# Kernel optimization log

Hardware: AMD Instinct MI355X
Metric: run time of the kernel (lower is better)

The kernel has to match this reference:

```python
import jax, jax.numpy as jnp
import numpy as np
from jax import lax

# Fixed-point scales (powers of two, as in linger's luna/venus pipeline).
# scale_gi = input_scale * weight_ih_scale, scale_gh = hidden_scale * weight_hh_scale.
SCALE_GI = 2.0 ** 14
SCALE_GH = 2.0 ** 14
Q27 = 2.0 ** 27
Q15 = 2.0 ** 15
Q31 = 2.0 ** 31
INT32_MIN = -(2.0 ** 31)
INT32_MAX = 2.0 ** 31 - 1


def quant_round(x, scale):
    # QuantMode.floor_add: floor(x*scale + 0.5)/scale, with straight-through gradient
    # (linger QAT rounding uses STE).
    q = jnp.floor(x * scale + 0.5) / scale
    return x + lax.stop_gradient(q - x)


@jax.custom_vjp
def qsigmoid(x):
    # Quantize input to Q27 int32, evaluate sigmoid, output Q31 -> requant to Q15.
    i_q27 = jnp.clip(jnp.floor(x * Q27 + 0.5), INT32_MIN, INT32_MAX)
    s = jax.nn.sigmoid(i_q27 / Q27)
    out_q31 = jnp.floor(s * Q31 + 0.5)
    out_q15 = jnp.floor(out_q31 * (2.0 ** -16) + 0.5)  # luna_requant(31 -> 15)
    return out_q15 / Q15

def _qsig_fwd(x):
    return qsigmoid(x), x

def _qsig_bwd(x, g):
    s = jax.nn.sigmoid(x)
    return (g * s * (1.0 - s),)

qsigmoid.defvjp(_qsig_fwd, _qsig_bwd)


@jax.custom_vjp
def qtanh(x):
    i_q27 = jnp.clip(jnp.floor(x * Q27 + 0.5), INT32_MIN, INT32_MAX)
    t = jnp.tanh(i_q27 / Q27)
    out_q31 = jnp.floor(t * Q31 + 0.5)
    out_q15 = jnp.floor(out_q31 * (2.0 ** -16) + 0.5)
    return out_q15 / Q15

def _qtanh_fwd(x):
    return qtanh(x), x

def _qtanh_bwd(x, g):
    t = jnp.tanh(x)
    return (g * (1.0 - t * t),)

qtanh.defvjp(_qtanh_fwd, _qtanh_bwd)


def setup_inputs() -> dict:
    key = jax.random.key(0)
    k = jax.random.split(key, 6)
    B, I, H = 8192, 512, 512
    return {
        "input_x": jax.random.normal(k[0], (B, I), dtype=jnp.float32),
        "hidden": jax.random.normal(k[1], (B, H), dtype=jnp.float32),
        "weight_ih": jax.random.normal(k[2], (3 * H, I), dtype=jnp.float32) * 0.05,
        "weight_hh": jax.random.normal(k[3], (3 * H, H), dtype=jnp.float32) * 0.05,
        "bias_ih": jax.random.normal(k[4], (3 * H,), dtype=jnp.float32) * 0.05,
        "bias_hh": jax.random.normal(k[5], (3 * H,), dtype=jnp.float32) * 0.05,
    }


def reference(input_x, hidden, weight_ih, weight_hh, bias_ih, bias_hh):
    # Dense gate projections: [B, 3H]
    gi = input_x @ weight_ih.T + bias_ih
    gh = hidden @ weight_hh.T + bias_hh
    # Requant gate pre-activations to fixed-point grid (biasih/biashh quantizers)
    gi = quant_round(gi, SCALE_GI)
    gh = quant_round(gh, SCALE_GH)
    i_r, i_i, i_n = jnp.split(gi, 3, axis=1)
    h_r, h_i, h_n = jnp.split(gh, 3, axis=1)
    resetgate = qsigmoid(i_r + h_r)
    inputgate = qsigmoid(i_i + h_i)
    # h_n requantized to Q27, reset*h_n product requantized to Q15
    h_n = quant_round(h_n, Q27)
    resetgate_h_n = quant_round(resetgate * h_n, Q15)
    newgate = qtanh(resetgate_h_n + i_n)
    new_hidden = quant_round(hidden, Q15)
    hy = newgate + inputgate * (new_hidden - newgate)
    return hy
```

## Files before the change

kernel.cpp:

```cpp
#include <hip/hip_runtime.h>
#include <math.h>


typedef _Float16 f16x8  __attribute__((ext_vector_type(8)));
typedef _Float16 f16x4  __attribute__((ext_vector_type(4)));
typedef __bf16   bf16x8 __attribute__((ext_vector_type(8)));
typedef float    f32x16 __attribute__((ext_vector_type(16)));

namespace {

constexpr int Bsz = 8192, Ksz = 512, Hsz = 512;
constexpr int BM = 64, BN = 64;

constexpr unsigned WCH0    = 16384u;
constexpr unsigned NCHUNK  = 16384u + 3072u;
constexpr unsigned WS_F16  = NCHUNK * 512u;
constexpr size_t   WS_NEED = (size_t)WS_F16 * 2;

__device__ __forceinline__ float qround(float x, float s, float invs) {
    return floorf(x * s + 0.5f) * invs;
}

__device__ __forceinline__ float qsigmoid_dev(float x) {
    float iq = floorf(x * 134217728.0f + 0.5f);
    iq = fminf(fmaxf(iq, -2147483648.0f), 2147483648.0f);
    float e = __expf(-iq * 7.450580596923828125e-9f);
    float s = __builtin_amdgcn_rcpf(1.0f + e);
    float q31 = floorf(s * 2147483648.0f + 0.5f);
    float q15 = floorf(q31 * 1.52587890625e-5f + 0.5f);
    return q15 * 3.0517578125e-5f;
}

__device__ __forceinline__ float qtanh_dev(float x) {
    float iq = floorf(x * 134217728.0f + 0.5f);
    iq = fminf(fmaxf(iq, -2147483648.0f), 2147483648.0f);
    float z = iq * 7.450580596923828125e-9f;
    float e = __expf(2.0f * z);
    float t = 1.0f - 2.0f * __builtin_amdgcn_rcpf(e + 1.0f);
    float q31 = floorf(t * 2147483648.0f + 0.5f);
    float q15 = floorf(q31 * 1.52587890625e-5f + 0.5f);
    return q15 * 3.0517578125e-5f;
}

__device__ __forceinline__ void dma16(const void* g, void* l) {
    __builtin_amdgcn_global_load_lds(
        (const __attribute__((address_space(1))) unsigned int*)g,
        (__attribute__((address_space(3))) unsigned int*)l, 16, 0, 0);
}

__device__ __forceinline__ void split2(float a, float b, unsigned& hi, unsigned& lo) {
    unsigned ua = __float_as_uint(a); ua += 0x7fffu + ((ua >> 16) & 1u);
    unsigned ub = __float_as_uint(b); ub += 0x7fffu + ((ub >> 16) & 1u);
    hi = (ua >> 16) | (ub & 0xffff0000u);
    float ra = a - __uint_as_float(ua & 0xffff0000u);
    float rb = b - __uint_as_float(ub & 0xffff0000u);
    unsigned va = __float_as_uint(ra); va += 0x7fffu + ((va >> 16) & 1u);
    unsigned vb = __float_as_uint(rb); vb += 0x7fffu + ((vb >> 16) & 1u);
    lo = (va >> 16) | (vb & 0xffff0000u);
}

}

__global__ __launch_bounds__(256) void cvt_lds_f16(
    const float* __restrict__ x, const float* __restrict__ h,
    const float* __restrict__ wih, const float* __restrict__ whh,
    _Float16* __restrict__ ws)
{
    __shared__ __align__(16) _Float16 lt[8192];

    const int b2  = blockIdx.x;
    const int b   = b2 >> 1;
    const int kha = b2 & 1;
    const int tid = threadIdx.x;

    const float* src;
    unsigned chbase;
    if (b < 512) {
        const int arr = b >> 8, M32 = b & 255;
        src = (arr ? h : x) + (size_t)M32 * 32u * 512u;
        chbase = (unsigned)arr * 8192u + (unsigned)M32 * 32u;
    } else {
        const int w = b - 512;
        const int g = w >> 4, N32 = w & 15;
        const int rowLocal = (g % 3) * 512 + N32 * 32;
        src = (g < 3 ? wih : whh) + (size_t)rowLocal * 512u;
        chbase = WCH0 + (unsigned)((g * 16 + N32) * 32);
    }
    src += kha * 256;

#pragma unroll
    for (int rep = 0; rep < 8; ++rep) {
        const int idx = rep * 256 + tid;
        const int row = idx >> 6;
        const int q   = idx & 63;
        const float4 v = *(const float4*)(src + (size_t)row * 512 + q * 4);
        const int K16l = q >> 2;
        const int kh   = (q >> 1) & 1;
        const int half = (q & 1) * 4;
        const int rsw  = (row + (q >> 1)) & 31;
        f16x4 o;
        o[0] = (_Float16)v.x; o[1] = (_Float16)v.y;
        o[2] = (_Float16)v.z; o[3] = (_Float16)v.w;
        *(f16x4*)&lt[K16l * 512 + kh * 256 + rsw * 8 + half] = o;
    }
    __syncthreads();

    const int wid = tid >> 6, lane = tid & 63;
    const int kh  = lane >> 5, row = lane & 31;
#pragma unroll
    for (int cc = 0; cc < 4; ++cc) {
        const int K16l = wid * 4 + cc;
        const int rsw  = (row + 2 * K16l + kh) & 31;
        const f16x8 o = *(const f16x8*)&lt[K16l * 512 + kh * 256 + rsw * 8];
        *(f16x8*)(ws + (size_t)(chbase + (unsigned)(kha * 16 + K16l)) * 512u
                      + lane * 8) = o;
    }
}

__global__ __launch_bounds__(256, 2) void qgru_f16_dma4(
    const _Float16* __restrict__ ws, const float* __restrict__ hid,
    const float* __restrict__ bih, const float* __restrict__ bhh,
    float* __restrict__ out)
{
    __shared__ __align__(16) _Float16 lds[24576];

    const int t = threadIdx.x, lane = t & 63, wid = t >> 6;
    const int mt = wid >> 1, nt = wid & 1;

    const int bid = blockIdx.x;
    const int xcd = bid & 7, j = bid >> 3;
    const int xw  = xcd + 8 * (j & 7);
    const int yw  = j >> 3;
    const int m0  = xw * 128, n0 = yw * 64;

    unsigned goffW[6];
    int      ldstW[6];
#pragma unroll
    for (int c = 0; c < 6; ++c) {
        const int gi = wid * 6 + c;
        const int g = gi >> 2, n32 = (gi >> 1) & 1, ks2 = gi & 1;
        const unsigned ch = WCH0
            + (unsigned)((g * 16 + (n0 >> 5) + n32) * 32) + (unsigned)ks2;
        goffW[c] = ch * 1024u + (unsigned)lane * 16u;
        ldstW[c] = ((g * 2 + n32) * 2 + ks2) * 512;
    }

    unsigned offA[8];
#pragma unroll
    for (int i = 0; i < 8; ++i) {
        const int ks2 = i >> 2, arr = (i >> 1) & 1, mf = i & 1;
        const unsigned ch = (unsigned)arr * 8192u
            + (unsigned)((m0 >> 5) + mt * 2 + mf) * 32u + (unsigned)ks2;
        offA[i] = ch * 1024u + (unsigned)lane * 16u;
    }

    f32x16 acc[4][2];
#pragma unroll
    for (int cid = 0; cid < 4; ++cid)
#pragma unroll
        for (int mf = 0; mf < 2; ++mf)
#pragma unroll
            for (int i = 0; i < 16; ++i) acc[cid][mf][i] = 0.0f;

    const char* wsb = (const char*)ws;
    const int lr = lane & 31, lk8 = (lane >> 5) * 8;

    f16x8 aA[8], aB[8];

#pragma unroll
    for (int i = 0; i < 8; ++i)
        aA[i] = *(const f16x8*)(wsb + offA[i]);
#pragma unroll
    for (int c = 0; c < 6; ++c)
        dma16(wsb + goffW[c], &lds[ldstW[c]]);

#define STEP_MFMA(ACUR, SLAB)                                                  \
    _Pragma("unroll")                                                          \
    for (int ks2 = 0; ks2 < 2; ++ks2) {                                        \
        const int lfo = (SLAB) + ks2 * 512 + lk8 * 32 + lr * 8;                \
        _Pragma("unroll")                                                      \
        for (int g = 0; g < 6; ++g) {                                          \
            const f16x8 bv = *(const f16x8*)&lds[lfo + (g * 2 + nt) * 1024];   \
            const int cid = (g < 3) ? g : (g == 5 ? 3 : g - 3);                \
            const f16x8 a0 = (g < 3) ? ACUR[ks2 * 4 + 0] : ACUR[ks2 * 4 + 2];  \
            const f16x8 a1 = (g < 3) ? ACUR[ks2 * 4 + 1] : ACUR[ks2 * 4 + 3];  \
            acc[cid][0] = __builtin_amdgcn_mfma_f32_32x32x16_f16(              \
                              a0, bv, acc[cid][0], 0, 0, 0);                   \
            acc[cid][1] = __builtin_amdgcn_mfma_f32_32x32x16_f16(              \
                              a1, bv, acc[cid][1], 0, 0, 0);                   \
        }                                                                      \
    }

    for (int sp = 0; sp < 8; ++sp) {
        {
            const unsigned kb = (unsigned)(2 * sp + 1) * 2048u;
#pragma unroll
            for (int i = 0; i < 8; ++i)
                aB[i] = *(const f16x8*)(wsb + offA[i] + kb);
#pragma unroll
            for (int c = 0; c < 6; ++c)
                dma16(wsb + goffW[c] + kb, &lds[12288 + ldstW[c]]);
            asm volatile("s_waitcnt vmcnt(14)" ::: "memory");
            __builtin_amdgcn_s_barrier();
            __builtin_amdgcn_s_setprio(1);
            STEP_MFMA(aA, 0)
            __builtin_amdgcn_s_setprio(0);
            asm volatile("" ::: "memory");
            __builtin_amdgcn_s_barrier();
        }
        {
            if (sp < 7) {
                const unsigned kb = (unsigned)(2 * sp + 2) * 2048u;
#pragma unroll
                for (int i = 0; i < 8; ++i)
                    aA[i] = *(const f16x8*)(wsb + offA[i] + kb);
#pragma unroll
                for (int c = 0; c < 6; ++c)
                    dma16(wsb + goffW[c] + kb, &lds[ldstW[c]]);
                asm volatile("s_waitcnt vmcnt(14)" ::: "memory");
            } else {
                asm volatile("s_waitcnt vmcnt(0)" ::: "memory");
            }
            __builtin_amdgcn_s_barrier();
            __builtin_amdgcn_s_setprio(1);
            STEP_MFMA(aB, 12288)
            __builtin_amdgcn_s_setprio(0);
            asm volatile("" ::: "memory");
            __builtin_amdgcn_s_barrier();
        }
    }
#undef STEP_MFMA

    constexpr float S14 = 16384.0f,     I14 = 1.0f / 16384.0f;
    constexpr float S15 = 32768.0f,     I15 = 1.0f / 32768.0f;

    const int lh = lane >> 5, l32 = lane & 31;
    const int n = n0 + nt * 32 + l32;
    const float brc = bih[n] + bhh[n];
    const float bic = bih[n + 512] + bhh[n + 512];
    const float bnn = bih[n + 1024];
    const float cnn = bhh[n + 1024];

#pragma unroll
    for (int mf = 0; mf < 2; ++mf) {
#pragma unroll
        for (int r = 0; r < 16; ++r) {
            const int row = (r & 3) + 8 * (r >> 2) + 4 * lh;
            const int m   = m0 + mt * 64 + mf * 32 + row;
            const float hv = hid[(size_t)m * Hsz + n];
            const float rg  = qsigmoid_dev(qround(acc[0][mf][r] + brc, S14, I14));
            const float ig  = qsigmoid_dev(qround(acc[1][mf][r] + bic, S14, I14));
            const float gin = qround(acc[2][mf][r] + bnn, S14, I14);
            const float ghn = qround(acc[3][mf][r] + cnn, S14, I14);
            const float rh  = qround(rg * ghn, S15, I15);
            const float ng  = qtanh_dev(rh + gin);
            const float nh  = qround(hv, S15, I15);
            out[(size_t)m * Hsz + n] = ng + ig * (nh - ng);
        }
    }
}

__global__ __launch_bounds__(256, 2) void qgru_mfma_bf16x3(
    const float* __restrict__ x, const float* __restrict__ hid,
    const float* __restrict__ wih, const float* __restrict__ whh,
    const float* __restrict__ bih, const float* __restrict__ bhh,
    float* __restrict__ out)
{
    __shared__ __align__(16) unsigned short lds[16384];

    const int t = threadIdx.x, lane = t & 63, wid = t >> 6;
    const int mt = wid >> 1, nt = wid & 1;
    const int m0 = blockIdx.x * BM, n0 = blockIdx.y * BN;
    const int s_r = t >> 2, s_k = (t & 3) << 2;
    const int s_kh = s_k >> 3, s_j = s_k & 7, s_rt = s_r >> 5, s_r32 = s_r & 31;

    const float* gA[2];
    gA[0] = x   + (size_t)(m0 + s_r) * Ksz + s_k;
    gA[1] = hid + (size_t)(m0 + s_r) * Ksz + s_k;
    const float* gW[6];
#pragma unroll
    for (int g = 0; g < 3; ++g) {
        gW[g]     = wih + (size_t)(g * Hsz + n0 + s_r) * Ksz + s_k;
        gW[g + 3] = whh + (size_t)(g * Hsz + n0 + s_r) * Ksz + s_k;
    }
    const int lh = lane >> 5, l32 = lane & 31;

    f32x16 acc[6];
#pragma unroll
    for (int g = 0; g < 6; ++g)
#pragma unroll
        for (int i = 0; i < 16; ++i) acc[g][i] = 0.0f;

    float4 vA[2], vW[6];
#pragma unroll
    for (int tt = 0; tt < 2; ++tt) vA[tt] = *(const float4*)gA[tt];
#pragma unroll
    for (int g = 0; g < 6; ++g)    vW[g]  = *(const float4*)gW[g];

    for (int k0 = 0; k0 < Ksz; k0 += 16) {
        __syncthreads();
#pragma unroll
        for (int tt = 0; tt < 2; ++tt) {
            unsigned h0, h1, l0, l1;
            split2(vA[tt].x, vA[tt].y, h0, l0);
            split2(vA[tt].z, vA[tt].w, h1, l1);
            unsigned bH = ((((tt*2+0)*2+s_rt)*2+s_kh)*32+s_r32)*8 + s_j;
            unsigned bL = ((((tt*2+1)*2+s_rt)*2+s_kh)*32+s_r32)*8 + s_j;
            *reinterpret_cast<uint2*>(&lds[bH]) = make_uint2(h0, h1);
            *reinterpret_cast<uint2*>(&lds[bL]) = make_uint2(l0, l1);
        }
#pragma unroll
        for (int g = 0; g < 6; ++g) {
            unsigned h0, h1, l0, l1;
            split2(vW[g].x, vW[g].y, h0, l0);
            split2(vW[g].z, vW[g].w, h1, l1);
            unsigned bH = 4096u + ((((g*2+0)*2+s_rt)*2+s_kh)*32+s_r32)*8 + s_j;
            unsigned bL = 4096u + ((((g*2+1)*2+s_rt)*2+s_kh)*32+s_r32)*8 + s_j;
            *reinterpret_cast<uint2*>(&lds[bH]) = make_uint2(h0, h1);
            *reinterpret_cast<uint2*>(&lds[bL]) = make_uint2(l0, l1);
        }
        __syncthreads();
        const int kn = (k0 + 16 < Ksz) ? (k0 + 16) : 0;
#pragma unroll
        for (int tt = 0; tt < 2; ++tt) vA[tt] = *(const float4*)(gA[tt] + kn);
#pragma unroll
        for (int g = 0; g < 6; ++g)    vW[g]  = *(const float4*)(gW[g] + kn);

        const bf16x8 ax_hi = *reinterpret_cast<const bf16x8*>(&lds[((((0)*2+mt)*2+lh)*32+l32)*8]);
        const bf16x8 ax_lo = *reinterpret_cast<const bf16x8*>(&lds[((((1)*2+mt)*2+lh)*32+l32)*8]);
        const bf16x8 ah_hi = *reinterpret_cast<const bf16x8*>(&lds[((((2)*2+mt)*2+lh)*32+l32)*8]);
        const bf16x8 ah_lo = *reinterpret_cast<const bf16x8*>(&lds[((((3)*2+mt)*2+lh)*32+l32)*8]);
#pragma unroll
        for (int g = 0; g < 6; ++g) {
            const bf16x8 b_hi = *reinterpret_cast<const bf16x8*>(&lds[4096u + ((((g*2+0)*2+nt)*2+lh)*32+l32)*8]);
            const bf16x8 b_lo = *reinterpret_cast<const bf16x8*>(&lds[4096u + ((((g*2+1)*2+nt)*2+lh)*32+l32)*8]);
            const bf16x8 a_hi = (g < 3) ? ax_hi : ah_hi;
            const bf16x8 a_lo = (g < 3) ? ax_lo : ah_lo;
            acc[g] = __builtin_amdgcn_mfma_f32_32x32x16_bf16(a_hi, b_hi, acc[g], 0, 0, 0);
            acc[g] = __builtin_amdgcn_mfma_f32_32x32x16_bf16(a_hi, b_lo, acc[g], 0, 0, 0);
            acc[g] = __builtin_amdgcn_mfma_f32_32x32x16_bf16(a_lo, b_hi, acc[g], 0, 0, 0);
        }
    }

    constexpr float S14 = 16384.0f,     I14 = 1.0f / 16384.0f;
    constexpr float S15 = 32768.0f,     I15 = 1.0f / 32768.0f;
    constexpr float S27 = 134217728.0f, I27 = 1.0f / 134217728.0f;
    const int n = n0 + nt * 32 + l32;
    const float br = bih[n], bi = bih[n + 512], bn = bih[n + 1024];
    const float cr = bhh[n], ci = bhh[n + 512], cn = bhh[n + 1024];
#pragma unroll
    for (int r = 0; r < 16; ++r) {
        const int row = (r & 3) + 8 * (r >> 2) + 4 * lh;
        const int m   = m0 + mt * 32 + row;
        const float hv = hid[(size_t)m * Hsz + n];
        float gir = qround(acc[0][r] + br, S14, I14);
        float gii = qround(acc[1][r] + bi, S14, I14);
        float gin = qround(acc[2][r] + bn, S14, I14);
        float ghr = qround(acc[3][r] + cr, S14, I14);
        float ghi = qround(acc[4][r] + ci, S14, I14);
        float ghn = qround(acc[5][r] + cn, S14, I14);
        float resetg = qsigmoid_dev(gir + ghr);
        float inputg = qsigmoid_dev(gii + ghi);
        float hn  = qround(ghn, S27, I27);
        float rh  = qround(resetg * hn, S15, I15);
        float newg = qtanh_dev(rh + gin);
        float nh  = qround(hv, S15, I15);
        out[(size_t)m * Hsz + n] = newg + inputg * (nh - newg);
    }
}

extern "C" void kernel_launch(void* const* d_in, const int* in_sizes, int n_in,
                              void* d_out, int out_size, void* d_ws, size_t ws_size,
                              hipStream_t stream) {
    const float* x   = (const float*)d_in[0];
    const float* hid = (const float*)d_in[1];
    const float* wih = (const float*)d_in[2];
    const float* whh = (const float*)d_in[3];
    const float* bih = (const float*)d_in[4];
    const float* bhh = (const float*)d_in[5];
    float* out = (float*)d_out;

    if (ws_size >= WS_NEED) {
        cvt_lds_f16<<<1216, 256, 0, stream>>>(
            x, hid, wih, whh, (_Float16*)d_ws);
        qgru_f16_dma4<<<512, 256, 0, stream>>>(
            (const _Float16*)d_ws, hid, bih, bhh, out);
    } else {
        dim3 grid(Bsz / BM, Hsz / BN);
        qgru_mfma_bf16x3<<<grid, dim3(256), 0, stream>>>(
            x, hid, wih, whh, bih, bhh, out);
    }
}
```

Measured before the change: 129.0 us.

## Use 512-thread blocks with 256-row tiles and triple-buffered K pipeline

```diff
diff --git a/kernel.cpp b/kernel.cpp
--- a/kernel.cpp
+++ b/kernel.cpp
@@ -16,6 +16,8 @@
 constexpr unsigned NCHUNK  = 16384u + 3072u;
 constexpr unsigned WS_F16  = NCHUNK * 512u;
 constexpr size_t   WS_NEED = (size_t)WS_F16 * 2;
+
+constexpr int SLAB = 14336;
 
 __device__ __forceinline__ float qround(float x, float s, float invs) {
     return floorf(x * s + 0.5f) * invs;
@@ -117,27 +119,25 @@
     }
 }
 
-__global__ __launch_bounds__(256, 2) void qgru_f16_dma4(
+__global__ __launch_bounds__(512, 2) void qgru_f16_dma5(
     const _Float16* __restrict__ ws, const float* __restrict__ hid,
     const float* __restrict__ bih, const float* __restrict__ bhh,
     float* __restrict__ out)
 {
-    __shared__ __align__(16) _Float16 lds[24576];
+    __shared__ __align__(16) _Float16 lds[3 * SLAB];
 
     const int t = threadIdx.x, lane = t & 63, wid = t >> 6;
     const int mt = wid >> 1, nt = wid & 1;
 
     const int bid = blockIdx.x;
-    const int xcd = bid & 7, j = bid >> 3;
-    const int xw  = xcd + 8 * (j & 7);
-    const int yw  = j >> 3;
-    const int m0  = xw * 128, n0 = yw * 64;
-
-    unsigned goffW[6];
-    int      ldstW[6];
-#pragma unroll
-    for (int c = 0; c < 6; ++c) {
-        const int gi = wid * 6 + c;
+    const int n0  = (bid & 7) * 64;
+    const int m0  = (bid >> 3) * 256;
+
+    unsigned goffW[3];
+    int      ldstW[3];
+#pragma unroll
+    for (int c = 0; c < 3; ++c) {
+        const int gi = wid * 3 + c;
         const int g = gi >> 2, n32 = (gi >> 1) & 1, ks2 = gi & 1;
         const unsigned ch = WCH0
             + (unsigned)((g * 16 + (n0 >> 5) + n32) * 32) + (unsigned)ks2;
@@ -165,71 +165,60 @@
     const char* wsb = (const char*)ws;
     const int lr = lane & 31, lk8 = (lane >> 5) * 8;
 
-    f16x8 aA[8], aB[8];
-
-#pragma unroll
-    for (int i = 0; i < 8; ++i)
-        aA[i] = *(const f16x8*)(wsb + offA[i]);
-#pragma unroll
-    for (int c = 0; c < 6; ++c)
-        dma16(wsb + goffW[c], &lds[ldstW[c]]);
-
-#define STEP_MFMA(ACUR, SLAB)                                                  \
-    _Pragma("unroll")                                                          \
-    for (int ks2 = 0; ks2 < 2; ++ks2) {                                        \
-        const int lfo = (SLAB) + ks2 * 512 + lk8 * 32 + lr * 8;                \
-        _Pragma("unroll")                                                      \
-        for (int g = 0; g < 6; ++g) {                                          \
-            const f16x8 bv = *(const f16x8*)&lds[lfo + (g * 2 + nt) * 1024];   \
-            const int cid = (g < 3) ? g : (g == 5 ? 3 : g - 3);                \
-            const f16x8 a0 = (g < 3) ? ACUR[ks2 * 4 + 0] : ACUR[ks2 * 4 + 2];  \
-            const f16x8 a1 = (g < 3) ? ACUR[ks2 * 4 + 1] : ACUR[ks2 * 4 + 3];  \
-            acc[cid][0] = __builtin_amdgcn_mfma_f32_32x32x16_f16(              \
-                              a0, bv, acc[cid][0], 0, 0, 0);                   \
-            acc[cid][1] = __builtin_amdgcn_mfma_f32_32x32x16_f16(              \
-                              a1, bv, acc[cid][1], 0, 0, 0);                   \
-        }                                                                      \
-    }
-
-    for (int sp = 0; sp < 8; ++sp) {
-        {
-            const unsigned kb = (unsigned)(2 * sp + 1) * 2048u;
+    f16x8 aS[3][8];
+
+#pragma unroll
+    for (int b = 0; b < 2; ++b) {
+        const unsigned kb = (unsigned)b * 2048u;
+#pragma unroll
+        for (int i = 0; i < 8; ++i)
+            aS[b][i] = *(const f16x8*)(wsb + offA[i] + kb);
+#pragma unroll
+        for (int c = 0; c < 3; ++c)
+            dma16(wsb + goffW[c] + kb, &lds[b * SLAB + ldstW[c]]);
+    }
+
+#pragma unroll
+    for (int step = 0; step < 16; ++step) {
+        const int cur = step % 3;
+
+        if (step < 14) {
+            const int nxt = (step + 2) % 3;
+            const unsigned kb = (unsigned)(step + 2) * 2048u;
 #pragma unroll
             for (int i = 0; i < 8; ++i)
-                aB[i] = *(const f16x8*)(wsb + offA[i] + kb);
-#pragma unroll
-            for (int c = 0; c < 6; ++c)
-                dma16(wsb + goffW[c] + kb, &lds[12288 + ldstW[c]]);
-            asm volatile("s_waitcnt vmcnt(14)" ::: "memory");
-            __builtin_amdgcn_s_barrier();
-            __builtin_amdgcn_s_setprio(1);
-            STEP_MFMA(aA, 0)
-            __builtin_amdgcn_s_setprio(0);
-            asm volatile("" ::: "memory");
-            __builtin_amdgcn_s_barrier();
-        }
-        {
-            if (sp < 7) {
-                const unsigned kb = (unsigned)(2 * sp + 2) * 2048u;
-#pragma unroll
-                for (int i = 0; i < 8; ++i)
-                    aA[i] = *(const f16x8*)(wsb + offA[i] + kb);
-#pragma unroll
-                for (int c = 0; c < 6; ++c)
-                    dma16(wsb + goffW[c] + kb, &lds[ldstW[c]]);
-                asm volatile("s_waitcnt vmcnt(14)" ::: "memory");
-            } else {
-                asm volatile("s_waitcnt vmcnt(0)" ::: "memory");
+                aS[nxt][i] = *(const f16x8*)(wsb + offA[i] + kb);
+#pragma unroll
+            for (int c = 0; c < 3; ++c)
+                dma16(wsb + goffW[c] + kb, &lds[nxt * SLAB + ldstW[c]]);
+            asm volatile("s_waitcnt vmcnt(22)" ::: "memory");
+        } else if (step == 14) {
+            asm volatile("s_waitcnt vmcnt(11)" ::: "memory");
+        } else {
+            asm volatile("s_waitcnt vmcnt(0)" ::: "memory");
+        }
+        __builtin_amdgcn_s_barrier();
+        __builtin_amdgcn_s_setprio(1);
+
+#pragma unroll
+        for (int ks2 = 0; ks2 < 2; ++ks2) {
+            const int lfo = cur * SLAB + ks2 * 512 + lk8 * 32 + lr * 8;
+#pragma unroll
+            for (int g = 0; g < 6; ++g) {
+                const f16x8 bv = *(const f16x8*)&lds[lfo + (g * 2 + nt) * 1024];
+                const int cid = (g < 3) ? g : (g == 5 ? 3 : g - 3);
+                const int ab  = ks2 * 4 + ((g < 3) ? 0 : 2);
+                acc[cid][0] = __builtin_amdgcn_mfma_f32_32x32x16_f16(
+                                  aS[cur][ab + 0], bv, acc[cid][0], 0, 0, 0);
+                acc[cid][1] = __builtin_amdgcn_mfma_f32_32x32x16_f16(
+                                  aS[cur][ab + 1], bv, acc[cid][1], 0, 0, 0);
             }
-            __builtin_amdgcn_s_barrier();
-            __builtin_amdgcn_s_setprio(1);
-            STEP_MFMA(aB, 12288)
-            __builtin_amdgcn_s_setprio(0);
-            asm volatile("" ::: "memory");
-            __builtin_amdgcn_s_barrier();
-        }
-    }
-#undef STEP_MFMA
+        }
+
+        __builtin_amdgcn_s_setprio(0);
+        asm volatile("" ::: "memory");
+        __builtin_amdgcn_s_barrier();
+    }
 
     constexpr float S14 = 16384.0f,     I14 = 1.0f / 16384.0f;
     constexpr float S15 = 32768.0f,     I15 = 1.0f / 32768.0f;
@@ -383,7 +372,7 @@
     if (ws_size >= WS_NEED) {
         cvt_lds_f16<<<1216, 256, 0, stream>>>(
             x, hid, wih, whh, (_Float16*)d_ws);
-        qgru_f16_dma4<<<512, 256, 0, stream>>>(
+        qgru_f16_dma5<<<256, 512, 0, stream>>>(
             (const _Float16*)d_ws, hid, bih, bhh, out);
     } else {
         dim3 grid(Bsz / BM, Hsz / BN);
```

Measured after the change: 129.9 us. No clear change (+0.7%).
